# Optimization experiments

Hardware: AMD Instinct MI355X
Metric: run time of the kernel (lower is better)

The kernel has to match this reference:

```python
import jax, jax.numpy as jnp
import numpy as np

B, EH, T = 8, 768, 512
PH, U = 320, 128
JH, C = 320, 34


def setup_inputs() -> dict:
    key = jax.random.key(0)
    ks = jax.random.split(key, 8)
    s_enc = 1.0 / np.sqrt(EH)
    s_pred = 1.0 / np.sqrt(PH)
    s_out = 1.0 / np.sqrt(JH)
    return {
        "enc": jax.random.normal(ks[0], (B, EH, T), dtype=jnp.float32),
        "dec": jax.random.normal(ks[1], (B, PH, U), dtype=jnp.float32),
        "W_enc": jax.random.normal(ks[2], (JH, EH), dtype=jnp.float32) * s_enc,
        "b_enc": jax.random.normal(ks[3], (JH,), dtype=jnp.float32) * s_enc,
        "W_pred": jax.random.normal(ks[4], (JH, PH), dtype=jnp.float32) * s_pred,
        "b_pred": jax.random.normal(ks[5], (JH,), dtype=jnp.float32) * s_pred,
        "W_out": jax.random.normal(ks[6], (C, JH), dtype=jnp.float32) * s_out,
        "b_out": jax.random.normal(ks[7], (C,), dtype=jnp.float32) * s_out,
    }


def reference(enc, dec, W_enc, b_enc, W_pred, b_pred, W_out, b_out):
    # enc: (B, EH, T) channels-first -> project each frame: (B, T, JH)
    e = jnp.einsum("bht,jh->btj", enc, W_enc) + b_enc
    # dec: (B, PH, U) -> (B, U, JH)
    p = jnp.einsum("bhu,ju->buj".replace("u,ju", "u,jh").replace("bhu", "bhu"), dec, W_pred) + b_pred if False else jnp.einsum("bhu,jh->buj", dec, W_pred) + b_pred
    # broadcast sum -> (B, T, U, JH), ReLU, small linear, log_softmax over classes
    h = jax.nn.relu(e[:, :, None, :] + p[:, None, :, :])
    logits = jnp.einsum("btuj,cj->btuc", h, W_out) + b_out
    return jax.nn.log_softmax(logits, axis=-1)
```

## Files before the change

### kernel.cpp

```cpp
#include <hip/hip_runtime.h>

#define B_ 8
#define EH_ 768
#define T_ 512
#define PH_ 320
#define U_ 128
#define JH_ 320
#define C_ 34
#define TTJ 8
#define LDP 328

typedef _Float16 f16x8 __attribute__((ext_vector_type(8)));
typedef _Float16 f16x4 __attribute__((ext_vector_type(4)));
typedef float f32x4 __attribute__((ext_vector_type(4)));

template <int CTRL>
static __device__ __forceinline__ float dpp_mov(float x) {
    int xi = __builtin_bit_cast(int, x);
    return __builtin_bit_cast(float, __builtin_amdgcn_update_dpp(xi, xi, CTRL, 0xf, 0xf, true));
}
static __device__ __forceinline__ float red16_max(float x) {
    x = fmaxf(x, dpp_mov<0xB1>(x));
    x = fmaxf(x, dpp_mov<0x4E>(x));
    x = fmaxf(x, dpp_mov<0x141>(x));
    x = fmaxf(x, dpp_mov<0x140>(x));
    return x;
}
static __device__ __forceinline__ float red16_sum(float x) {
    x += dpp_mov<0xB1>(x);
    x += dpp_mov<0x4E>(x);
    x += dpp_mov<0x141>(x);
    x += dpp_mov<0x140>(x);
    return x;
}

static __device__ __forceinline__ f16x8 relu_sum8(f16x8 a, f16x8 b) {
    f16x8 s = a + b;
    f16x8 z = (f16x8)(_Float16)0.f;
    return __builtin_elementwise_max(s, z);
}

__global__ __launch_bounds__(256) void transpose_cvt_kernel(
    const float* __restrict__ src, _Float16* __restrict__ dst, int H, int N)
{
    __shared__ _Float16 tile[32][36];
    const int tid = threadIdx.x;
    const int tx = tid & 7, ty = tid >> 3;
    const int n0 = blockIdx.x * 32, h0 = blockIdx.y * 32, b = blockIdx.z;

    float4 v = *(const float4*)&src[((size_t)b * H + h0 + ty) * N + n0 + tx * 4];
    f16x4 t;
    t[0] = (_Float16)v.x; t[1] = (_Float16)v.y; t[2] = (_Float16)v.z; t[3] = (_Float16)v.w;
    *(f16x4*)&tile[ty][tx * 4] = t;
    __syncthreads();

    f16x4 o;
    o[0] = tile[tx * 4 + 0][ty];
    o[1] = tile[tx * 4 + 1][ty];
    o[2] = tile[tx * 4 + 2][ty];
    o[3] = tile[tx * 4 + 3][ty];
    *(f16x4*)&dst[((size_t)b * N + n0 + ty) * H + h0 + tx * 4] = o;
}

__global__ void weights_cvt_kernel(
    const float* __restrict__ Wenc, const float* __restrict__ Wpred,
    const float* __restrict__ Wout,
    _Float16* __restrict__ wenc, _Float16* __restrict__ wpred, _Float16* __restrict__ wout)
{
    const int t1 = JH_ * EH_, t2 = JH_ * PH_, t3 = 48 * JH_;
    int i = blockIdx.x * 256 + threadIdx.x;
    if (i < t1) {
        wenc[i] = (_Float16)Wenc[i];
    } else if (i < t1 + t2) {
        wpred[i - t1] = (_Float16)Wpred[i - t1];
    } else if (i < t1 + t2 + t3) {
        int k = i - t1 - t2;
        int c = k / JH_;
        wout[k] = (c < C_) ? (_Float16)Wout[k] : (_Float16)0.f;
    }
}

__global__ __launch_bounds__(256) void proj_direct_kernel(
    const _Float16* __restrict__ src_t, const _Float16* __restrict__ Wf,
    const float* __restrict__ bias, _Float16* __restrict__ dst, int H, int N)
{
    const int tid = threadIdx.x;
    const int wave = tid >> 6, lane = tid & 63;
    const int lrow = lane & 15, quad = lane >> 4;
    const int ntn = N / 32;

    int gid = blockIdx.x * 4 + wave;
    const int nt_ = gid % ntn; gid /= ntn;
    const int jt_ = gid % (JH_ / 32);
    const int b   = gid / (JH_ / 32);
    const int n0 = nt_ * 32, j0 = jt_ * 32;

    const _Float16* a0p = src_t + ((size_t)b * N + n0 + lrow) * H + quad * 8;
    const _Float16* a1p = a0p + (size_t)16 * H;
    const _Float16* w0p = Wf + (size_t)(j0 + lrow) * H + quad * 8;
    const _Float16* w1p = w0p + (size_t)16 * H;

    f32x4 acc00 = {0.f,0.f,0.f,0.f}, acc01 = {0.f,0.f,0.f,0.f};
    f32x4 acc10 = {0.f,0.f,0.f,0.f}, acc11 = {0.f,0.f,0.f,0.f};

#pragma unroll 2
    for (int k = 0; k < H; k += 32) {
        f16x8 a0 = *(const f16x8*)(a0p + k);
        f16x8 a1 = *(const f16x8*)(a1p + k);
        f16x8 w0 = *(const f16x8*)(w0p + k);
        f16x8 w1 = *(const f16x8*)(w1p + k);
        acc00 = __builtin_amdgcn_mfma_f32_16x16x32_f16(a0, w0, acc00, 0, 0, 0);
        acc01 = __builtin_amdgcn_mfma_f32_16x16x32_f16(a0, w1, acc01, 0, 0, 0);
        acc10 = __builtin_amdgcn_mfma_f32_16x16x32_f16(a1, w0, acc10, 0, 0, 0);
        acc11 = __builtin_amdgcn_mfma_f32_16x16x32_f16(a1, w1, acc11, 0, 0, 0);
    }

    const float bj0 = bias[j0 + lrow];
    const float bj1 = bias[j0 + 16 + lrow];
#pragma unroll
    for (int nt = 0; nt < 2; ++nt) {
        const f32x4 ac0 = nt ? acc10 : acc00;
        const f32x4 ac1 = nt ? acc11 : acc01;
#pragma unroll
        for (int i = 0; i < 4; ++i) {
            const int n = n0 + nt * 16 + quad * 4 + i;
            _Float16* d = dst + ((size_t)b * N + n) * JH_ + j0;
            d[lrow]      = (_Float16)(ac0[i] + bj0);
            d[16 + lrow] = (_Float16)(ac1[i] + bj1);
        }
    }
}

__global__ __launch_bounds__(256) void joint_kernel(
    const _Float16* __restrict__ e_f, const _Float16* __restrict__ p_f,
    const _Float16* __restrict__ wout_f, const float* __restrict__ b_out,
    float* __restrict__ out)
{
    __shared__ alignas(16) _Float16 p_lds[64 * LDP];
    __shared__ alignas(16) _Float16 w_lds[48 * LDP];
    __shared__ alignas(16) _Float16 e_lds[TTJ * LDP];

    const int tid = threadIdx.x;
    const int t0  = blockIdx.x * TTJ;
    const int u0  = blockIdx.y * 64;
    const int b   = blockIdx.z;

    {
        const uint4* sp = (const uint4*)(p_f + ((size_t)b * U_ + u0) * JH_);
        for (int i = tid; i < 64 * 40; i += 256) {
            int r = i / 40, k8 = i % 40;
            *(uint4*)&p_lds[r * LDP + k8 * 8] = sp[i];
        }
        const uint4* sw = (const uint4*)wout_f;
        for (int i = tid; i < 48 * 40; i += 256) {
            int r = i / 40, k8 = i % 40;
            *(uint4*)&w_lds[r * LDP + k8 * 8] = sw[i];
        }
        const uint4* se = (const uint4*)(e_f + ((size_t)b * T_ + t0) * JH_);
        for (int i = tid; i < TTJ * 40; i += 256) {
            int r = i / 40, k8 = i % 40;
            *(uint4*)&e_lds[r * LDP + k8 * 8] = se[i];
        }
    }
    __syncthreads();

    const int lane = tid & 63;
    const int wave = tid >> 6;
    const int lrow = lane & 15;
    const int quad = lane >> 4;
    const int lk   = quad * 8;
    const int arow = wave * 16 + lrow;

    const bool v2 = (lrow < 2);
    const float bo0 = b_out[lrow];
    const float bo1 = b_out[16 + lrow];
    const float bo2 = v2 ? b_out[32 + lrow] : 0.f;

    f32x4 acc[TTJ][3];
#pragma unroll
    for (int tt = 0; tt < TTJ; ++tt)
#pragma unroll
        for (int nt = 0; nt < 3; ++nt)
            acc[tt][nt] = (f32x4){0.f, 0.f, 0.f, 0.f};

    for (int kk = 0; kk < 10; ++kk) {
        const int k = lk + kk * 32;
        f16x8 pv = *(const f16x8*)&p_lds[arow * LDP + k];
        f16x8 w0 = *(const f16x8*)&w_lds[(0 * 16 + lrow) * LDP + k];
        f16x8 w1 = *(const f16x8*)&w_lds[(1 * 16 + lrow) * LDP + k];
        f16x8 w2 = *(const f16x8*)&w_lds[(2 * 16 + lrow) * LDP + k];
#pragma unroll
        for (int tt = 0; tt < TTJ; ++tt) {
            f16x8 ev = *(const f16x8*)&e_lds[tt * LDP + k];
            f16x8 h = relu_sum8(pv, ev);
            acc[tt][0] = __builtin_amdgcn_mfma_f32_16x16x32_f16(h, w0, acc[tt][0], 0, 0, 0);
            acc[tt][1] = __builtin_amdgcn_mfma_f32_16x16x32_f16(h, w1, acc[tt][1], 0, 0, 0);
            acc[tt][2] = __builtin_amdgcn_mfma_f32_16x16x32_f16(h, w2, acc[tt][2], 0, 0, 0);
        }
    }

#pragma unroll
    for (int tt = 0; tt < TTJ; ++tt) {
        const size_t rowbase = ((size_t)b * T_ + (t0 + tt)) * U_ + u0 + wave * 16;
#pragma unroll
        for (int i = 0; i < 4; ++i) {
            const int rl = quad * 4 + i;
            float v0  = acc[tt][0][i] + bo0;
            float v1  = acc[tt][1][i] + bo1;
            float vv2 = v2 ? (acc[tt][2][i] + bo2) : -INFINITY;
            float m = red16_max(fmaxf(fmaxf(v0, v1), vv2));
            float s = __expf(v0 - m) + __expf(v1 - m) + (v2 ? __expf(vv2 - m) : 0.f);
            s = red16_sum(s);
            const float lse = m + __logf(s);
            float* po = out + (rowbase + rl) * C_;
            po[lrow]      = v0 - lse;
            po[16 + lrow] = v1 - lse;
            if (v2) po[32 + lrow] = vv2 - lse;
        }
    }
}

extern "C" void kernel_launch(void* const* d_in, const int* in_sizes, int n_in,
                              void* d_out, int out_size, void* d_ws, size_t ws_size,
                              hipStream_t stream) {
    const float* enc    = (const float*)d_in[0];
    const float* dec    = (const float*)d_in[1];
    const float* W_enc  = (const float*)d_in[2];
    const float* b_enc  = (const float*)d_in[3];
    const float* W_pred = (const float*)d_in[4];
    const float* b_pred = (const float*)d_in[5];
    const float* W_out  = (const float*)d_in[6];
    const float* b_out  = (const float*)d_in[7];
    float* out = (float*)d_out;

    _Float16* enc_t  = (_Float16*)d_ws;
    _Float16* dec_t  = enc_t  + (size_t)B_ * T_ * EH_;
    _Float16* wenc_f = dec_t  + (size_t)B_ * U_ * PH_;
    _Float16* wpred_f= wenc_f + (size_t)JH_ * EH_;
    _Float16* wout_f = wpred_f+ (size_t)JH_ * PH_;
    _Float16* e_f    = wout_f + (size_t)48 * JH_;
    _Float16* p_f    = e_f    + (size_t)B_ * T_ * JH_;

    transpose_cvt_kernel<<<dim3(T_ / 32, EH_ / 32, B_), 256, 0, stream>>>(enc, enc_t, EH_, T_);
    transpose_cvt_kernel<<<dim3(U_ / 32, PH_ / 32, B_), 256, 0, stream>>>(dec, dec_t, PH_, U_);
    weights_cvt_kernel<<<dim3((JH_ * EH_ + JH_ * PH_ + 48 * JH_ + 255) / 256), 256, 0, stream>>>(
        W_enc, W_pred, W_out, wenc_f, wpred_f, wout_f);

    proj_direct_kernel<<<dim3((T_ / 32) * (JH_ / 32) * B_ / 4), 256, 0, stream>>>(
        enc_t, wenc_f, b_enc, e_f, EH_, T_);
    proj_direct_kernel<<<dim3((U_ / 32) * (JH_ / 32) * B_ / 4), 256, 0, stream>>>(
        dec_t, wpred_f, b_pred, p_f, PH_, U_);

    joint_kernel<<<dim3(T_ / TTJ, 2, B_), 256, 0, stream>>>(e_f, p_f, wout_f, b_out, out);
}
```

Baseline: 166.5 us.

## Merge prep and projection launches, retile joint kernel with transposed MFMA outputs

The two transposes and the weight conversion are folded into one prep kernel, and the two projection GEMMs into one launch. This removes launch gaps and lets the small dec and weight work share the GPU with the enc work. Projections now use one 16x16 tile per wave with the weight as the A operand, so bias loads and output stores are vectorized. The joint kernel is retiled to 32 u by 8 t per block, with the weights padded to 34 rows instead of 48 and all tiles in one LDS buffer. Swapping the MFMA operands lets each lane hold a row's classes, so log-softmax reduces with two shuffles and writes float2 stores; the trade-off is more blocks, each reloading the weights.

```diff
diff --git a/kernel.cpp b/kernel.cpp
--- a/kernel.cpp
+++ b/kernel.cpp
@@ -7,32 +7,11 @@
 #define U_ 128
 #define JH_ 320
 #define C_ 34
-#define TTJ 8
 #define LDP 328
 
 typedef _Float16 f16x8 __attribute__((ext_vector_type(8)));
 typedef _Float16 f16x4 __attribute__((ext_vector_type(4)));
 typedef float f32x4 __attribute__((ext_vector_type(4)));
-
-template <int CTRL>
-static __device__ __forceinline__ float dpp_mov(float x) {
-    int xi = __builtin_bit_cast(int, x);
-    return __builtin_bit_cast(float, __builtin_amdgcn_update_dpp(xi, xi, CTRL, 0xf, 0xf, true));
-}
-static __device__ __forceinline__ float red16_max(float x) {
-    x = fmaxf(x, dpp_mov<0xB1>(x));
-    x = fmaxf(x, dpp_mov<0x4E>(x));
-    x = fmaxf(x, dpp_mov<0x141>(x));
-    x = fmaxf(x, dpp_mov<0x140>(x));
-    return x;
-}
-static __device__ __forceinline__ float red16_sum(float x) {
-    x += dpp_mov<0xB1>(x);
-    x += dpp_mov<0x4E>(x);
-    x += dpp_mov<0x141>(x);
-    x += dpp_mov<0x140>(x);
-    return x;
-}
 
 static __device__ __forceinline__ f16x8 relu_sum8(f16x8 a, f16x8 b) {
     f16x8 s = a + b;
@@ -40,95 +19,89 @@
     return __builtin_elementwise_max(s, z);
 }
 
-__global__ __launch_bounds__(256) void transpose_cvt_kernel(
-    const float* __restrict__ src, _Float16* __restrict__ dst, int H, int N)
+__global__ __launch_bounds__(256) void prep_kernel(
+    const float* __restrict__ enc, const float* __restrict__ dec,
+    const float* __restrict__ Wenc, const float* __restrict__ Wpred,
+    const float* __restrict__ Wout,
+    _Float16* __restrict__ enc_t, _Float16* __restrict__ dec_t,
+    _Float16* __restrict__ wenc, _Float16* __restrict__ wpred,
+    _Float16* __restrict__ wout)
 {
     __shared__ _Float16 tile[32][36];
+    const int NE = 16 * 24 * B_;
+    const int ND = 4 * 10 * B_;
     const int tid = threadIdx.x;
-    const int tx = tid & 7, ty = tid >> 3;
-    const int n0 = blockIdx.x * 32, h0 = blockIdx.y * 32, b = blockIdx.z;
-
-    float4 v = *(const float4*)&src[((size_t)b * H + h0 + ty) * N + n0 + tx * 4];
-    f16x4 t;
-    t[0] = (_Float16)v.x; t[1] = (_Float16)v.y; t[2] = (_Float16)v.z; t[3] = (_Float16)v.w;
-    *(f16x4*)&tile[ty][tx * 4] = t;
-    __syncthreads();
-
-    f16x4 o;
-    o[0] = tile[tx * 4 + 0][ty];
-    o[1] = tile[tx * 4 + 1][ty];
-    o[2] = tile[tx * 4 + 2][ty];
-    o[3] = tile[tx * 4 + 3][ty];
-    *(f16x4*)&dst[((size_t)b * N + n0 + ty) * H + h0 + tx * 4] = o;
-}
-
-__global__ void weights_cvt_kernel(
-    const float* __restrict__ Wenc, const float* __restrict__ Wpred,
-    const float* __restrict__ Wout,
-    _Float16* __restrict__ wenc, _Float16* __restrict__ wpred, _Float16* __restrict__ wout)
-{
-    const int t1 = JH_ * EH_, t2 = JH_ * PH_, t3 = 48 * JH_;
-    int i = blockIdx.x * 256 + threadIdx.x;
-    if (i < t1) {
-        wenc[i] = (_Float16)Wenc[i];
-    } else if (i < t1 + t2) {
-        wpred[i - t1] = (_Float16)Wpred[i - t1];
-    } else if (i < t1 + t2 + t3) {
-        int k = i - t1 - t2;
-        int c = k / JH_;
-        wout[k] = (c < C_) ? (_Float16)Wout[k] : (_Float16)0.f;
-    }
-}
-
-__global__ __launch_bounds__(256) void proj_direct_kernel(
-    const _Float16* __restrict__ src_t, const _Float16* __restrict__ Wf,
-    const float* __restrict__ bias, _Float16* __restrict__ dst, int H, int N)
+    int bid = blockIdx.x;
+
+    if (bid < NE + ND) {
+        const float* src; _Float16* dst; int H, N, n0, h0, b;
+        if (bid < NE) {
+            src = enc; dst = enc_t; H = EH_; N = T_;
+            n0 = (bid % 16) * 32; h0 = ((bid / 16) % 24) * 32; b = bid / (16 * 24);
+        } else {
+            int i = bid - NE;
+            src = dec; dst = dec_t; H = PH_; N = U_;
+            n0 = (i % 4) * 32; h0 = ((i / 4) % 10) * 32; b = i / 40;
+        }
+        const int tx = tid & 7, ty = tid >> 3;
+        float4 v = *(const float4*)&src[((size_t)b * H + h0 + ty) * N + n0 + tx * 4];
+        f16x4 t;
+        t[0] = (_Float16)v.x; t[1] = (_Float16)v.y; t[2] = (_Float16)v.z; t[3] = (_Float16)v.w;
+        *(f16x4*)&tile[ty][tx * 4] = t;
+        __syncthreads();
+        f16x4 o;
+        o[0] = tile[tx * 4 + 0][ty];
+        o[1] = tile[tx * 4 + 1][ty];
+        o[2] = tile[tx * 4 + 2][ty];
+        o[3] = tile[tx * 4 + 3][ty];
+        *(f16x4*)&dst[((size_t)b * N + n0 + ty) * H + h0 + tx * 4] = o;
+    } else {
+        const int t1 = JH_ * EH_, t2 = JH_ * PH_, t3 = C_ * JH_;
+        int i = (bid - NE - ND) * 256 + tid;
+        if (i < t1)                wenc[i] = (_Float16)Wenc[i];
+        else if (i < t1 + t2)      wpred[i - t1] = (_Float16)Wpred[i - t1];
+        else if (i < t1 + t2 + t3) wout[i - t1 - t2] = (_Float16)Wout[i - t1 - t2];
+    }
+}
+
+__global__ __launch_bounds__(256) void proj_kernel(
+    const _Float16* __restrict__ enc_t, const _Float16* __restrict__ dec_t,
+    const _Float16* __restrict__ wenc, const _Float16* __restrict__ wpred,
+    const float* __restrict__ b_enc, const float* __restrict__ b_pred,
+    _Float16* __restrict__ e_f, _Float16* __restrict__ p_f)
 {
     const int tid = threadIdx.x;
     const int wave = tid >> 6, lane = tid & 63;
     const int lrow = lane & 15, quad = lane >> 4;
-    const int ntn = N / 32;
-
-    int gid = blockIdx.x * 4 + wave;
-    const int nt_ = gid % ntn; gid /= ntn;
-    const int jt_ = gid % (JH_ / 32);
-    const int b   = gid / (JH_ / 32);
-    const int n0 = nt_ * 32, j0 = jt_ * 32;
-
-    const _Float16* a0p = src_t + ((size_t)b * N + n0 + lrow) * H + quad * 8;
-    const _Float16* a1p = a0p + (size_t)16 * H;
-    const _Float16* w0p = Wf + (size_t)(j0 + lrow) * H + quad * 8;
-    const _Float16* w1p = w0p + (size_t)16 * H;
-
-    f32x4 acc00 = {0.f,0.f,0.f,0.f}, acc01 = {0.f,0.f,0.f,0.f};
-    f32x4 acc10 = {0.f,0.f,0.f,0.f}, acc11 = {0.f,0.f,0.f,0.f};
-
-#pragma unroll 2
+
+    int wid = blockIdx.x * 4 + wave;
+    const int We = (T_ / 16) * (JH_ / 16) * B_;
+    const _Float16 *src, *W; const float* bias; _Float16* dst; int H, N;
+    if (wid < We) { src = enc_t; W = wenc;  bias = b_enc;  dst = e_f; H = EH_; N = T_; }
+    else { wid -= We; src = dec_t; W = wpred; bias = b_pred; dst = p_f; H = PH_; N = U_; }
+
+    const int ntn = N / 16;
+    const int nt = wid % ntn; int r = wid / ntn;
+    const int jt = r % (JH_ / 16); const int b = r / (JH_ / 16);
+    const int n0 = nt * 16, j0 = jt * 16;
+
+    const _Float16* ap = src + ((size_t)b * N + n0 + lrow) * H + quad * 8;
+    const _Float16* wp = W + (size_t)(j0 + lrow) * H + quad * 8;
+
+    f32x4 acc = {0.f, 0.f, 0.f, 0.f};
+#pragma unroll 4
     for (int k = 0; k < H; k += 32) {
-        f16x8 a0 = *(const f16x8*)(a0p + k);
-        f16x8 a1 = *(const f16x8*)(a1p + k);
-        f16x8 w0 = *(const f16x8*)(w0p + k);
-        f16x8 w1 = *(const f16x8*)(w1p + k);
-        acc00 = __builtin_amdgcn_mfma_f32_16x16x32_f16(a0, w0, acc00, 0, 0, 0);
-        acc01 = __builtin_amdgcn_mfma_f32_16x16x32_f16(a0, w1, acc01, 0, 0, 0);
-        acc10 = __builtin_amdgcn_mfma_f32_16x16x32_f16(a1, w0, acc10, 0, 0, 0);
-        acc11 = __builtin_amdgcn_mfma_f32_16x16x32_f16(a1, w1, acc11, 0, 0, 0);
-    }
-
-    const float bj0 = bias[j0 + lrow];
-    const float bj1 = bias[j0 + 16 + lrow];
-#pragma unroll
-    for (int nt = 0; nt < 2; ++nt) {
-        const f32x4 ac0 = nt ? acc10 : acc00;
-        const f32x4 ac1 = nt ? acc11 : acc01;
-#pragma unroll
-        for (int i = 0; i < 4; ++i) {
-            const int n = n0 + nt * 16 + quad * 4 + i;
-            _Float16* d = dst + ((size_t)b * N + n) * JH_ + j0;
-            d[lrow]      = (_Float16)(ac0[i] + bj0);
-            d[16 + lrow] = (_Float16)(ac1[i] + bj1);
-        }
-    }
+        f16x8 af = *(const f16x8*)(ap + k);
+        f16x8 wf = *(const f16x8*)(wp + k);
+        acc = __builtin_amdgcn_mfma_f32_16x16x32_f16(wf, af, acc, 0, 0, 0);
+    }
+    const float4 bj = *(const float4*)&bias[j0 + quad * 4];
+    f16x4 o;
+    o[0] = (_Float16)(acc[0] + bj.x);
+    o[1] = (_Float16)(acc[1] + bj.y);
+    o[2] = (_Float16)(acc[2] + bj.z);
+    o[3] = (_Float16)(acc[3] + bj.w);
+    *(f16x4*)&dst[((size_t)b * N + n0 + lrow) * JH_ + j0 + quad * 4] = o;
 }
 
 __global__ __launch_bounds__(256) void joint_kernel(
@@ -136,87 +109,97 @@
     const _Float16* __restrict__ wout_f, const float* __restrict__ b_out,
     float* __restrict__ out)
 {
-    __shared__ alignas(16) _Float16 p_lds[64 * LDP];
-    __shared__ alignas(16) _Float16 w_lds[48 * LDP];
-    __shared__ alignas(16) _Float16 e_lds[TTJ * LDP];
+    __shared__ alignas(16) _Float16 lds[(34 + 32 + 8) * LDP];
 
     const int tid = threadIdx.x;
-    const int t0  = blockIdx.x * TTJ;
-    const int u0  = blockIdx.y * 64;
-    const int b   = blockIdx.z;
+    const int t0 = blockIdx.x * 8;
+    const int u0 = blockIdx.y * 32;
+    const int b  = blockIdx.z;
 
     {
+        const uint4* sw = (const uint4*)wout_f;
+        for (int i = tid; i < 34 * 40; i += 256) {
+            int rr = i / 40, k8 = i % 40;
+            *(uint4*)&lds[rr * LDP + k8 * 8] = sw[i];
+        }
         const uint4* sp = (const uint4*)(p_f + ((size_t)b * U_ + u0) * JH_);
-        for (int i = tid; i < 64 * 40; i += 256) {
-            int r = i / 40, k8 = i % 40;
-            *(uint4*)&p_lds[r * LDP + k8 * 8] = sp[i];
-        }
-        const uint4* sw = (const uint4*)wout_f;
-        for (int i = tid; i < 48 * 40; i += 256) {
-            int r = i / 40, k8 = i % 40;
-            *(uint4*)&w_lds[r * LDP + k8 * 8] = sw[i];
+        for (int i = tid; i < 32 * 40; i += 256) {
+            int rr = i / 40, k8 = i % 40;
+            *(uint4*)&lds[(34 + rr) * LDP + k8 * 8] = sp[i];
         }
         const uint4* se = (const uint4*)(e_f + ((size_t)b * T_ + t0) * JH_);
-        for (int i = tid; i < TTJ * 40; i += 256) {
-            int r = i / 40, k8 = i % 40;
-            *(uint4*)&e_lds[r * LDP + k8 * 8] = se[i];
+        for (int i = tid; i < 8 * 40; i += 256) {
+            int rr = i / 40, k8 = i % 40;
+            *(uint4*)&lds[(66 + rr) * LDP + k8 * 8] = se[i];
         }
     }
     __syncthreads();
 
-    const int lane = tid & 63;
-    const int wave = tid >> 6;
-    const int lrow = lane & 15;
-    const int quad = lane >> 4;
-    const int lk   = quad * 8;
-    const int arow = wave * 16 + lrow;
-
-    const bool v2 = (lrow < 2);
-    const float bo0 = b_out[lrow];
-    const float bo1 = b_out[16 + lrow];
-    const float bo2 = v2 ? b_out[32 + lrow] : 0.f;
-
-    f32x4 acc[TTJ][3];
-#pragma unroll
-    for (int tt = 0; tt < TTJ; ++tt)
-#pragma unroll
-        for (int nt = 0; nt < 3; ++nt)
-            acc[tt][nt] = (f32x4){0.f, 0.f, 0.f, 0.f};
+    const int lane = tid & 63, wave = tid >> 6;
+    const int lrow = lane & 15, quad = lane >> 4;
+    const int lk = quad * 8;
+    const int urow  = 34 + (wave & 1) * 16 + lrow;
+    const int tbase = 66 + (wave >> 1) * 4;
+
+    f32x4 acc[4][3];
+#pragma unroll
+    for (int tt = 0; tt < 4; ++tt)
+#pragma unroll
+        for (int c = 0; c < 3; ++c) acc[tt][c] = (f32x4){0.f, 0.f, 0.f, 0.f};
 
     for (int kk = 0; kk < 10; ++kk) {
         const int k = lk + kk * 32;
-        f16x8 pv = *(const f16x8*)&p_lds[arow * LDP + k];
-        f16x8 w0 = *(const f16x8*)&w_lds[(0 * 16 + lrow) * LDP + k];
-        f16x8 w1 = *(const f16x8*)&w_lds[(1 * 16 + lrow) * LDP + k];
-        f16x8 w2 = *(const f16x8*)&w_lds[(2 * 16 + lrow) * LDP + k];
-#pragma unroll
-        for (int tt = 0; tt < TTJ; ++tt) {
-            f16x8 ev = *(const f16x8*)&e_lds[tt * LDP + k];
+        f16x8 pv = *(const f16x8*)&lds[urow * LDP + k];
+        f16x8 w0 = *(const f16x8*)&lds[(0  + lrow) * LDP + k];
+        f16x8 w1 = *(const f16x8*)&lds[(16 + lrow) * LDP + k];
+        f16x8 w2 = *(const f16x8*)&lds[(32 + lrow) * LDP + k];
+#pragma unroll
+        for (int tt = 0; tt < 4; ++tt) {
+            f16x8 ev = *(const f16x8*)&lds[(tbase + tt) * LDP + k];
             f16x8 h = relu_sum8(pv, ev);
-            acc[tt][0] = __builtin_amdgcn_mfma_f32_16x16x32_f16(h, w0, acc[tt][0], 0, 0, 0);
-            acc[tt][1] = __builtin_amdgcn_mfma_f32_16x16x32_f16(h, w1, acc[tt][1], 0, 0, 0);
-            acc[tt][2] = __builtin_amdgcn_mfma_f32_16x16x32_f16(h, w2, acc[tt][2], 0, 0, 0);
-        }
-    }
-
-#pragma unroll
-    for (int tt = 0; tt < TTJ; ++tt) {
-        const size_t rowbase = ((size_t)b * T_ + (t0 + tt)) * U_ + u0 + wave * 16;
-#pragma unroll
-        for (int i = 0; i < 4; ++i) {
-            const int rl = quad * 4 + i;
-            float v0  = acc[tt][0][i] + bo0;
-            float v1  = acc[tt][1][i] + bo1;
-            float vv2 = v2 ? (acc[tt][2][i] + bo2) : -INFINITY;
-            float m = red16_max(fmaxf(fmaxf(v0, v1), vv2));
-            float s = __expf(v0 - m) + __expf(v1 - m) + (v2 ? __expf(vv2 - m) : 0.f);
-            s = red16_sum(s);
-            const float lse = m + __logf(s);
-            float* po = out + (rowbase + rl) * C_;
-            po[lrow]      = v0 - lse;
-            po[16 + lrow] = v1 - lse;
-            if (v2) po[32 + lrow] = vv2 - lse;
-        }
+            acc[tt][0] = __builtin_amdgcn_mfma_f32_16x16x32_f16(w0, h, acc[tt][0], 0, 0, 0);
+            acc[tt][1] = __builtin_amdgcn_mfma_f32_16x16x32_f16(w1, h, acc[tt][1], 0, 0, 0);
+            acc[tt][2] = __builtin_amdgcn_mfma_f32_16x16x32_f16(w2, h, acc[tt][2], 0, 0, 0);
+        }
+    }
+
+    const float4 bq0 = *(const float4*)&b_out[quad * 4];
+    const float4 bq1 = *(const float4*)&b_out[16 + quad * 4];
+    const bool q0 = (quad == 0);
+    float b2x = 0.f, b2y = 0.f;
+    if (q0) { b2x = b_out[32]; b2y = b_out[33]; }
+
+    const int u = u0 + (wave & 1) * 16 + lrow;
+#pragma unroll
+    for (int tt = 0; tt < 4; ++tt) {
+        float v0[4], v1[4];
+        v0[0] = acc[tt][0][0] + bq0.x; v0[1] = acc[tt][0][1] + bq0.y;
+        v0[2] = acc[tt][0][2] + bq0.z; v0[3] = acc[tt][0][3] + bq0.w;
+        v1[0] = acc[tt][1][0] + bq1.x; v1[1] = acc[tt][1][1] + bq1.y;
+        v1[2] = acc[tt][1][2] + bq1.z; v1[3] = acc[tt][1][3] + bq1.w;
+        float v2x = q0 ? (acc[tt][2][0] + b2x) : -INFINITY;
+        float v2y = q0 ? (acc[tt][2][1] + b2y) : -INFINITY;
+
+        float m = fmaxf(fmaxf(fmaxf(v0[0], v0[1]), fmaxf(v0[2], v0[3])),
+                        fmaxf(fmaxf(v1[0], v1[1]), fmaxf(v1[2], v1[3])));
+        m = fmaxf(m, fmaxf(v2x, v2y));
+        m = fmaxf(m, __shfl_xor(m, 16));
+        m = fmaxf(m, __shfl_xor(m, 32));
+
+        float s = __expf(v0[0] - m) + __expf(v0[1] - m) + __expf(v0[2] - m) + __expf(v0[3] - m)
+                + __expf(v1[0] - m) + __expf(v1[1] - m) + __expf(v1[2] - m) + __expf(v1[3] - m);
+        if (q0) s += __expf(v2x - m) + __expf(v2y - m);
+        s += __shfl_xor(s, 16);
+        s += __shfl_xor(s, 32);
+        const float lse = m + __logf(s);
+
+        const int t = t0 + (wave >> 1) * 4 + tt;
+        float* po = out + (((size_t)b * T_ + t) * U_ + u) * C_;
+        *(float2*)&po[quad * 4]          = make_float2(v0[0] - lse, v0[1] - lse);
+        *(float2*)&po[quad * 4 + 2]      = make_float2(v0[2] - lse, v0[3] - lse);
+        *(float2*)&po[16 + quad * 4]     = make_float2(v1[0] - lse, v1[1] - lse);
+        *(float2*)&po[16 + quad * 4 + 2] = make_float2(v1[2] - lse, v1[3] - lse);
+        if (q0) *(float2*)&po[32]        = make_float2(v2x - lse, v2y - lse);
     }
 }
 
@@ -238,18 +221,18 @@
     _Float16* wenc_f = dec_t  + (size_t)B_ * U_ * PH_;
     _Float16* wpred_f= wenc_f + (size_t)JH_ * EH_;
     _Float16* wout_f = wpred_f+ (size_t)JH_ * PH_;
-    _Float16* e_f    = wout_f + (size_t)48 * JH_;
+    _Float16* e_f    = wout_f + (size_t)C_ * JH_;
     _Float16* p_f    = e_f    + (size_t)B_ * T_ * JH_;
 
-    transpose_cvt_kernel<<<dim3(T_ / 32, EH_ / 32, B_), 256, 0, stream>>>(enc, enc_t, EH_, T_);
-    transpose_cvt_kernel<<<dim3(U_ / 32, PH_ / 32, B_), 256, 0, stream>>>(dec, dec_t, PH_, U_);
-    weights_cvt_kernel<<<dim3((JH_ * EH_ + JH_ * PH_ + 48 * JH_ + 255) / 256), 256, 0, stream>>>(
-        W_enc, W_pred, W_out, wenc_f, wpred_f, wout_f);
-
-    proj_direct_kernel<<<dim3((T_ / 32) * (JH_ / 32) * B_ / 4), 256, 0, stream>>>(
-        enc_t, wenc_f, b_enc, e_f, EH_, T_);
-    proj_direct_kernel<<<dim3((U_ / 32) * (JH_ / 32) * B_ / 4), 256, 0, stream>>>(
-        dec_t, wpred_f, b_pred, p_f, PH_, U_);
-
-    joint_kernel<<<dim3(T_ / TTJ, 2, B_), 256, 0, stream>>>(e_f, p_f, wout_f, b_out, out);
-}
+    const int NE = 16 * 24 * B_, ND = 4 * 10 * B_;
+    const int NW = (JH_ * EH_ + JH_ * PH_ + C_ * JH_ + 255) / 256;
+    prep_kernel<<<dim3(NE + ND + NW), 256, 0, stream>>>(
+        enc, dec, W_enc, W_pred, W_out, enc_t, dec_t, wenc_f, wpred_f, wout_f);
+
+    const int We = (T_ / 16) * (JH_ / 16) * B_;
+    const int Wp = (U_ / 16) * (JH_ / 16) * B_;
+    proj_kernel<<<dim3((We + Wp) / 4), 256, 0, stream>>>(
+        enc_t, dec_t, wenc_f, wpred_f, b_enc, b_pred, e_f, p_f);
+
+    joint_kernel<<<dim3(T_ / 8, U_ / 32, B_), 256, 0, stream>>>(e_f, p_f, wout_f, b_out, out);
+}
```

Result: faster. 153.0 us (-8.1%).
